# Kernel tuning notes

Measured on AMD Instinct MI355X. Metric: run time of the kernel, lower is better.

Reference implementation:

```python
import jax, jax.numpy as jnp
import numpy as np

HIDDEN = 192
NUM_LAYERS = 5
ATOMS_PER_MOL = 8
B = 200000
N = B * ATOMS_PER_MOL
EPS = 1e-5  # torch LayerNorm default


def setup_inputs() -> dict:
    key = jax.random.key(0)
    ks = jax.random.split(key, 12)
    z = jax.random.randint(ks[0], (N,), 1, 104, dtype=jnp.int32)
    pos = jax.random.normal(ks[1], (N, 3), dtype=jnp.float32) * 3.0
    batch = (jnp.arange(N, dtype=jnp.int32) // ATOMS_PER_MOL)  # sorted, 8 atoms/molecule
    emb = jax.random.normal(ks[2], (104, HIDDEN), dtype=jnp.float32) * 0.02
    layer_W = jax.random.normal(ks[3], (NUM_LAYERS, HIDDEN, HIDDEN), dtype=jnp.float32) * 0.05
    layer_b = jnp.zeros((NUM_LAYERS, HIDDEN), dtype=jnp.float32)
    layer_g = jnp.ones((NUM_LAYERS, HIDDEN), dtype=jnp.float32)
    layer_beta = jnp.zeros((NUM_LAYERS, HIDDEN), dtype=jnp.float32)
    dist_W = jax.random.normal(ks[4], (HIDDEN, 1), dtype=jnp.float32) * 0.05
    dist_b = jnp.zeros((HIDDEN,), dtype=jnp.float32)
    head_W1 = jax.random.normal(ks[5], (HIDDEN, 3 * HIDDEN), dtype=jnp.float32) * 0.05
    head_b1 = jnp.zeros((HIDDEN,), dtype=jnp.float32)
    head_W2 = jax.random.normal(ks[6], (1, HIDDEN), dtype=jnp.float32) * 0.05
    head_b2 = jnp.zeros((1,), dtype=jnp.float32)
    images = jnp.zeros((1,), dtype=jnp.float32)  # ignored by the model
    return {
        "images": images, "z": z, "pos": pos, "batch": batch,
        "num_molecules": B,
        "emb": emb, "layer_W": layer_W, "layer_b": layer_b,
        "layer_g": layer_g, "layer_beta": layer_beta,
        "dist_W": dist_W, "dist_b": dist_b,
        "head_W1": head_W1, "head_b1": head_b1,
        "head_W2": head_W2, "head_b2": head_b2,
    }


def _layer_norm(y, g, b):
    mu = y.mean(-1, keepdims=True)
    var = y.var(-1, keepdims=True)  # biased, matches torch LayerNorm
    return (y - mu) * jax.lax.rsqrt(var + EPS) * g + b


def _tower(h, layer_W, layer_b, layer_g, layer_beta):
    # residual: h = h + Dropout(ReLU(LN(Linear(h)))); dropout = identity (eval)
    for i in range(layer_W.shape[0]):
        y = h @ layer_W[i].T + layer_b[i]
        h = h + jax.nn.relu(_layer_norm(y, layer_g[i], layer_beta[i]))
    return h


def reference(images, z, pos, batch, num_molecules, emb, layer_W, layer_b,
              layer_g, layer_beta, dist_W, dist_b, head_W1, head_b1,
              head_W2, head_b2):
    Bm = int(num_molecules)
    mol_ids = jnp.arange(Bm, dtype=batch.dtype)
    # batch is sorted -> first atom index of each molecule
    first = jnp.searchsorted(batch, mol_ids)
    counts = jax.ops.segment_sum(jnp.ones_like(batch), batch, num_segments=Bm)
    has2 = counts > 1
    second = jnp.where(has2, first + 1, first)

    h1 = emb[z[first]]   # [B, H]
    h2 = emb[z[second]]  # [B, H]
    h1 = _tower(h1, layer_W, layer_b, layer_g, layer_beta)
    h2 = _tower(h2, layer_W, layer_b, layer_g, layer_beta)

    diff = pos[first] - pos[second]
    dist = jnp.sqrt(jnp.sum(diff * diff, axis=-1) + 1e-12)  # [B]
    dist = jnp.where(has2, dist, 0.0)
    dist_feat = dist[:, None] * dist_W[:, 0][None, :] + dist_b  # Linear(1, H)

    combined = jnp.concatenate([h1, h2, dist_feat], axis=-1)  # [B, 3H]
    x = jax.nn.relu(combined @ head_W1.T + head_b1)
    out = x @ head_W2.T + head_b2  # [B, 1]
    return out.squeeze(-1)
```

## Files before the change

kernel.cpp:

```cpp
#include <hip/hip_runtime.h>

#define H 192
#define NLAYERS 5
#define NTYPES 104
#define EPSLN 1e-5f
#define ATOMS 8


__device__ __forceinline__ float block_sum_3waves(float v, volatile float* red, int tid) {
  #pragma unroll
  for (int o = 32; o > 0; o >>= 1) v += __shfl_xor(v, o, 64);
  if ((tid & 63) == 0) red[tid >> 6] = v;
  __syncthreads();
  float s = red[0] + red[1] + red[2];
  __syncthreads();
  return s;
}

__global__ void build_tables_kernel(
    const float* __restrict__ emb, const float* __restrict__ layer_W,
    const float* __restrict__ layer_b, const float* __restrict__ layer_g,
    const float* __restrict__ layer_beta, const float* __restrict__ dist_W,
    const float* __restrict__ dist_b, const float* __restrict__ head_W1,
    const float* __restrict__ head_b1,
    float* __restrict__ U1, float* __restrict__ U2,
    float* __restrict__ cvec, float* __restrict__ dvec) {
  __shared__ __align__(16) float h[H];
  __shared__ float red[4];
  const int t = blockIdx.x;
  const int j = threadIdx.x;

  h[j] = emb[t * H + j];
  __syncthreads();

  const float4* h4 = reinterpret_cast<const float4*>(h);

  for (int L = 0; L < NLAYERS; ++L) {
    const float4* W4 = reinterpret_cast<const float4*>(layer_W + (L * H + j) * H);
    float acc = layer_b[L * H + j];
    #pragma unroll 4
    for (int k = 0; k < H / 4; ++k) {
      float4 hv = h4[k];
      float4 wv = W4[k];
      acc = fmaf(hv.x, wv.x, acc);
      acc = fmaf(hv.y, wv.y, acc);
      acc = fmaf(hv.z, wv.z, acc);
      acc = fmaf(hv.w, wv.w, acc);
    }
    float mu = block_sum_3waves(acc, red, j) * (1.0f / H);
    float dev = acc - mu;
    float var = block_sum_3waves(dev * dev, red, j) * (1.0f / H);
    float ln = dev * rsqrtf(var + EPSLN) * layer_g[L * H + j] + layer_beta[L * H + j];
    float hn = h[j] + fmaxf(ln, 0.0f);
    __syncthreads();
    h[j] = hn;
    __syncthreads();
  }

  const float4* w1a = reinterpret_cast<const float4*>(head_W1 + j * (3 * H));
  const float4* w1b = reinterpret_cast<const float4*>(head_W1 + j * (3 * H) + H);
  float a1 = 0.0f, a2 = 0.0f;
  #pragma unroll 4
  for (int k = 0; k < H / 4; ++k) {
    float4 hv = h4[k];
    float4 va = w1a[k];
    float4 vb = w1b[k];
    a1 = fmaf(hv.x, va.x, a1); a1 = fmaf(hv.y, va.y, a1);
    a1 = fmaf(hv.z, va.z, a1); a1 = fmaf(hv.w, va.w, a1);
    a2 = fmaf(hv.x, vb.x, a2); a2 = fmaf(hv.y, vb.y, a2);
    a2 = fmaf(hv.z, vb.z, a2); a2 = fmaf(hv.w, vb.w, a2);
  }
  U1[t * H + j] = a1;
  U2[t * H + j] = a2;

  if (t == 0) {
    const float4* w1c = reinterpret_cast<const float4*>(head_W1 + j * (3 * H) + 2 * H);
    const float4* dw4 = reinterpret_cast<const float4*>(dist_W);
    const float4* db4 = reinterpret_cast<const float4*>(dist_b);
    float cc = 0.0f, dd = head_b1[j];
    #pragma unroll 4
    for (int k = 0; k < H / 4; ++k) {
      float4 vc = w1c[k];
      float4 vw = dw4[k];
      float4 vb = db4[k];
      cc = fmaf(vw.x, vc.x, cc); cc = fmaf(vw.y, vc.y, cc);
      cc = fmaf(vw.z, vc.z, cc); cc = fmaf(vw.w, vc.w, cc);
      dd = fmaf(vb.x, vc.x, dd); dd = fmaf(vb.y, vc.y, dd);
      dd = fmaf(vb.z, vc.z, dd); dd = fmaf(vb.w, vc.w, dd);
    }
    cvec[j] = cc;
    dvec[j] = dd;
  }
}

__global__ __launch_bounds__(256) void mol_kernel(
    const int* __restrict__ z, const float* __restrict__ pos,
    const float* __restrict__ U1, const float* __restrict__ U2,
    const float* __restrict__ cvec, const float* __restrict__ dvec,
    const float* __restrict__ head_W2, const float* __restrict__ head_b2,
    float* __restrict__ out, int B) {
  const int l   = threadIdx.x & 31;
  const int hw  = (blockIdx.x << 3) | (threadIdx.x >> 5);
  const int nhw = gridDim.x << 3;

  float c0[6], d0[6], w2[6];
  #pragma unroll
  for (int r = 0; r < 6; ++r) {
    const int jj = l + (r << 5);
    c0[r] = cvec[jj];
    d0[r] = dvec[jj];
    w2[r] = head_W2[jj];
  }
  const float b2 = head_b2[0];

  for (int m = hw; m < B; m += nhw) {
    const int a0 = m << 3;
    const int2 zz  = *reinterpret_cast<const int2*>(z + a0);
    const float4 p0 = *reinterpret_cast<const float4*>(pos + a0 * 3);
    const float2 p1 = *reinterpret_cast<const float2*>(pos + a0 * 3 + 4);
    const float dx = p0.x - p0.w;
    const float dy = p0.y - p1.x;
    const float dz = p0.z - p1.y;
    const float dist = sqrtf(dx * dx + dy * dy + dz * dz + 1e-12f);

    const float* __restrict__ u1 = U1 + zz.x * H;
    const float* __restrict__ u2 = U2 + zz.y * H;

    float acc = 0.f;
    #pragma unroll
    for (int r = 0; r < 6; ++r) {
      const int jj = l + (r << 5);
      float x = u1[jj] + u2[jj] + fmaf(dist, c0[r], d0[r]);
      acc = fmaf(fmaxf(x, 0.f), w2[r], acc);
    }
    #pragma unroll
    for (int o = 16; o > 0; o >>= 1) acc += __shfl_xor(acc, o, 64);
    if (l == 0) out[m] = acc + b2;
  }
}

extern "C" void kernel_launch(void* const* d_in, const int* in_sizes, int n_in,
                              void* d_out, int out_size, void* d_ws, size_t ws_size,
                              hipStream_t stream) {
  const int*   z          = (const int*)  d_in[1];
  const float* pos        = (const float*)d_in[2];
  const float* emb        = (const float*)d_in[5];
  const float* layer_W    = (const float*)d_in[6];
  const float* layer_b    = (const float*)d_in[7];
  const float* layer_g    = (const float*)d_in[8];
  const float* layer_beta = (const float*)d_in[9];
  const float* dist_W     = (const float*)d_in[10];
  const float* dist_b     = (const float*)d_in[11];
  const float* head_W1    = (const float*)d_in[12];
  const float* head_b1    = (const float*)d_in[13];
  const float* head_W2    = (const float*)d_in[14];
  const float* head_b2    = (const float*)d_in[15];
  float* out = (float*)d_out;

  const int N = in_sizes[1];
  const int B = N / ATOMS;

  float* ws = (float*)d_ws;
  float* U1   = ws;
  float* U2   = U1 + NTYPES * H;
  float* cvec = U2 + NTYPES * H;
  float* dvec = cvec + H;

  build_tables_kernel<<<NTYPES, H, 0, stream>>>(
      emb, layer_W, layer_b, layer_g, layer_beta, dist_W, dist_b,
      head_W1, head_b1, U1, U2, cvec, dvec);

  mol_kernel<<<2048, 256, 0, stream>>>(z, pos, U1, U2, cvec, dvec,
                                       head_W2, head_b2, out, B);
}
```

Baseline: 166.9 us.

## Stage U1/U2 tables in LDS and relaunch mol kernel with 256 large blocks

The mol kernel now copies both per-type tables (2*104*192 floats, about 160KB) into dynamic shared memory once per block. The per-molecule gathers then read from LDS instead of global/L2. To amortize the copy it uses 256 blocks of 512 threads, and the table-build loops are fully unrolled with launch bounds set. The risks are the large per-block LDS copy, and the fact that only one block fits per CU, which limits occupancy and latency hiding for the z/pos streaming loads.

```diff
diff --git a/kernel.cpp b/kernel.cpp
--- a/kernel.cpp
+++ b/kernel.cpp
@@ -5,7 +5,8 @@
 #define NTYPES 104
 #define EPSLN 1e-5f
 #define ATOMS 8
-
+#define MOLBLK 512
+#define MOLGRID 256
 
 __device__ __forceinline__ float block_sum_3waves(float v, volatile float* red, int tid) {
   #pragma unroll
@@ -17,7 +18,7 @@
   return s;
 }
 
-__global__ void build_tables_kernel(
+__global__ __launch_bounds__(192, 1) void build_tables_kernel(
     const float* __restrict__ emb, const float* __restrict__ layer_W,
     const float* __restrict__ layer_b, const float* __restrict__ layer_g,
     const float* __restrict__ layer_beta, const float* __restrict__ dist_W,
@@ -38,7 +39,7 @@
   for (int L = 0; L < NLAYERS; ++L) {
     const float4* W4 = reinterpret_cast<const float4*>(layer_W + (L * H + j) * H);
     float acc = layer_b[L * H + j];
-    #pragma unroll 4
+    #pragma unroll
     for (int k = 0; k < H / 4; ++k) {
       float4 hv = h4[k];
       float4 wv = W4[k];
@@ -60,7 +61,7 @@
   const float4* w1a = reinterpret_cast<const float4*>(head_W1 + j * (3 * H));
   const float4* w1b = reinterpret_cast<const float4*>(head_W1 + j * (3 * H) + H);
   float a1 = 0.0f, a2 = 0.0f;
-  #pragma unroll 4
+  #pragma unroll
   for (int k = 0; k < H / 4; ++k) {
     float4 hv = h4[k];
     float4 va = w1a[k];
@@ -78,7 +79,7 @@
     const float4* dw4 = reinterpret_cast<const float4*>(dist_W);
     const float4* db4 = reinterpret_cast<const float4*>(dist_b);
     float cc = 0.0f, dd = head_b1[j];
-    #pragma unroll 4
+    #pragma unroll
     for (int k = 0; k < H / 4; ++k) {
       float4 vc = w1c[k];
       float4 vw = dw4[k];
@@ -93,15 +94,15 @@
   }
 }
 
-__global__ __launch_bounds__(256) void mol_kernel(
+__global__ __launch_bounds__(MOLBLK) void mol_kernel(
     const int* __restrict__ z, const float* __restrict__ pos,
-    const float* __restrict__ U1, const float* __restrict__ U2,
+    const float* __restrict__ U1 ,
     const float* __restrict__ cvec, const float* __restrict__ dvec,
     const float* __restrict__ head_W2, const float* __restrict__ head_b2,
     float* __restrict__ out, int B) {
-  const int l   = threadIdx.x & 31;
-  const int hw  = (blockIdx.x << 3) | (threadIdx.x >> 5);
-  const int nhw = gridDim.x << 3;
+  extern __shared__ __align__(16) float uls[];
+  const int tid = threadIdx.x;
+  const int l   = tid & 31;
 
   float c0[6], d0[6], w2[6];
   #pragma unroll
@@ -113,6 +114,16 @@
   }
   const float b2 = head_b2[0];
 
+  {
+    const float4* src = reinterpret_cast<const float4*>(U1);
+    float4* dst = reinterpret_cast<float4*>(uls);
+    for (int i = tid; i < (2 * NTYPES * H) / 4; i += MOLBLK) dst[i] = src[i];
+  }
+  __syncthreads();
+
+  const int hw  = (blockIdx.x << 4) | (tid >> 5);
+  const int nhw = gridDim.x << 4;
+
   for (int m = hw; m < B; m += nhw) {
     const int a0 = m << 3;
     const int2 zz  = *reinterpret_cast<const int2*>(z + a0);
@@ -123,8 +134,8 @@
     const float dz = p0.z - p1.y;
     const float dist = sqrtf(dx * dx + dy * dy + dz * dz + 1e-12f);
 
-    const float* __restrict__ u1 = U1 + zz.x * H;
-    const float* __restrict__ u2 = U2 + zz.y * H;
+    const float* u1 = uls + zz.x * H;
+    const float* u2 = uls + (NTYPES * H) + zz.y * H;
 
     float acc = 0.f;
     #pragma unroll
@@ -166,10 +177,14 @@
   float* cvec = U2 + NTYPES * H;
   float* dvec = cvec + H;
 
+  (void)hipFuncSetAttribute(reinterpret_cast<const void*>(mol_kernel),
+                            hipFuncAttributeMaxDynamicSharedMemorySize,
+                            2 * NTYPES * H * (int)sizeof(float));
+
   build_tables_kernel<<<NTYPES, H, 0, stream>>>(
       emb, layer_W, layer_b, layer_g, layer_beta, dist_W, dist_b,
       head_W1, head_b1, U1, U2, cvec, dvec);
 
-  mol_kernel<<<2048, 256, 0, stream>>>(z, pos, U1, U2, cvec, dvec,
-                                       head_W2, head_b2, out, B);
+  mol_kernel<<<MOLGRID, MOLBLK, 2 * NTYPES * H * sizeof(float), stream>>>(
+      z, pos, U1, cvec, dvec, head_W2, head_b2, out, B);
 }
```

Measured after the change: 181.7 us. +8.9%, slower.
